# Optimization experiments

Hardware: AMD Instinct MI355X
Metric: run time of the kernel (lower is better)

The kernel has to match this reference:

```python
import jax, jax.numpy as jnp
import numpy as np

N_NODES = 50000
N_EDGES = 800000
D_FEAT = 128
D_HID = 500


def setup_inputs() -> dict:
    key = jax.random.key(0)
    k1, k2, k3, k4 = jax.random.split(key, 4)
    x = jax.random.normal(k1, (N_NODES, D_FEAT), dtype=jnp.float32)
    edge_index = jax.random.randint(k2, (2, N_EDGES), 0, N_NODES, dtype=jnp.int64)
    # Glorot-ish init for weights, zeros for bias (PyG GCNConv default)
    W1 = jax.random.normal(k3, (D_FEAT, D_HID), dtype=jnp.float32) / np.sqrt(D_FEAT)
    b1 = jnp.zeros((D_HID,), dtype=jnp.float32)
    W2 = jax.random.normal(k4, (D_HID, 1), dtype=jnp.float32) / np.sqrt(D_HID)
    b2 = jnp.zeros((1,), dtype=jnp.float32)
    return {"x": x, "edge_index": edge_index, "W1": W1, "b1": b1, "W2": W2, "b2": b2}


def gcn_conv(x, W, b, src, dst, n_nodes):
    """PyG GCNConv: linear transform, add self-loops, symmetric norm, scatter-add, bias."""
    h = x @ W  # [N, out]
    loops = jnp.arange(n_nodes, dtype=src.dtype)
    s = jnp.concatenate([src, loops])  # [E+N]
    d = jnp.concatenate([dst, loops])
    deg = jnp.zeros((n_nodes,), dtype=h.dtype).at[d].add(1.0)
    dinv = jnp.where(deg > 0, jax.lax.rsqrt(deg), 0.0)
    norm = dinv[s] * dinv[d]  # [E+N]
    msg = h[s] * norm[:, None]  # [E+N, out] -- dominant memory traffic
    out = jax.ops.segment_sum(msg, d, num_segments=n_nodes)
    return out + b


def reference(x, edge_index, W1, b1, W2, b2):
    src, dst = edge_index[0], edge_index[1]
    n = x.shape[0]
    h = gcn_conv(x, W1, b1, src, dst, n)
    h = jax.nn.relu(h)
    # F.dropout(training=self.training): identity in eval mode
    out = gcn_conv(h, W2, b2, src, dst, n)
    return out
```

## Files before the change

### kernel.cpp

```cpp
#include <hip/hip_runtime.h>


#define N_NODES 50000
#define N_EDGES 800000
#define D_FEAT  128
#define D_HID   500
#define NTILES  3125
#define RB2     1563
#define CSTRIDE 64

typedef __bf16 bf16x8 __attribute__((ext_vector_type(8)));
typedef float  f32x4  __attribute__((ext_vector_type(4)));

static __device__ inline unsigned int f2bf(float f) {
    unsigned int u = __float_as_uint(f);
    return (u + 0x7fffu + ((u >> 16) & 1u)) >> 16;
}
static __device__ inline float bf_lo(unsigned int u) { return __uint_as_float(u << 16); }
static __device__ inline float bf_hi(unsigned int u) { return __uint_as_float(u & 0xffff0000u); }

static __device__ inline void add8(float* acc, uint4 u) {
    acc[0] += bf_lo(u.x);
    acc[1] += bf_hi(u.x);
    acc[2] += bf_lo(u.y);
    acc[3] += bf_hi(u.y);
    acc[4] += bf_lo(u.z);
    acc[5] += bf_hi(u.z);
    acc[6] += bf_lo(u.w);
    acc[7] += bf_hi(u.w);
}

__global__ __launch_bounds__(256) void k_rank(const int* __restrict__ dst,
                                              const float* __restrict__ W1,
                                              const float* __restrict__ b1,
                                              const float* __restrict__ W2,
                                              int* __restrict__ deg,
                                              int* __restrict__ rank,
                                              unsigned short* __restrict__ b_pk,
                                              float* __restrict__ b1p,
                                              float* __restrict__ w2p) {
    const int b = blockIdx.x, tid = threadIdx.x;
    if (b < RB2) {
        int t2 = b * 256 + tid;
        if (t2 < N_EDGES / 2) {
            int e = t2 * 2;
            int2 d2 = *(const int2*)&dst[e];
            int2 r2;
            r2.x = atomicAdd(&deg[d2.x], 1);
            r2.y = atomicAdd(&deg[d2.y], 1);
            *(int2*)&rank[e] = r2;
        }
    } else if (b < RB2 + 32) {
        int idx  = (b - RB2) * 256 + tid;
        int lane = idx & 63;
        int slot = idx >> 6;
        int t    = slot >> 2;
        int ks   = slot & 3;
        int quad = lane >> 4;
        int n    = t * 16 + (lane & 15);
        unsigned int us[8];
#pragma unroll
        for (int j = 0; j < 8; j++) {
            int k = ks * 32 + quad * 8 + j;
            float v = (n < D_HID) ? W1[(size_t)k * D_HID + n] : 0.f;
            us[j] = f2bf(v);
        }
        uint4 p;
        p.x = us[0] | (us[1] << 16);
        p.y = us[2] | (us[3] << 16);
        p.z = us[4] | (us[5] << 16);
        p.w = us[6] | (us[7] << 16);
        ((uint4*)b_pk)[idx] = p;
    } else {
        for (int i = tid; i < 512; i += 256) {
            b1p[i] = (i < D_HID) ? b1[i] : 0.f;
            w2p[i] = (i < D_HID) ? W2[i] : 0.f;
        }
    }
}

__global__ __launch_bounds__(256) void k_fill(const int* __restrict__ src,
                                              const int* __restrict__ dst,
                                              const int* __restrict__ rank,
                                              const int* __restrict__ deg,
                                              const float* __restrict__ x,
                                              unsigned short* __restrict__ csrp,
                                              uint2* __restrict__ xd) {
    const int e = blockIdx.x * 256 + threadIdx.x;
    {
        int r = rank[e];
        if (r < CSTRIDE)
            csrp[dst[e] * CSTRIDE + r] = (unsigned short)src[e];
    }
    for (int i = e; i < N_NODES * D_FEAT / 4; i += N_EDGES) {
        float d = rsqrtf((float)(deg[i >> 5] + 1));
        float4 v = ((const float4*)x)[i];
        uint2 o;
        o.x = f2bf(d * v.x) | (f2bf(d * v.y) << 16);
        o.y = f2bf(d * v.z) | (f2bf(d * v.w) << 16);
        xd[i] = o;
    }
}

__global__ __launch_bounds__(256, 8) void k_gcn1(const uint4* __restrict__ xd4,
                                                 const unsigned short* __restrict__ csrp,
                                                 const int* __restrict__ deg,
                                                 const unsigned short* __restrict__ b_pk,
                                                 const float* __restrict__ b1p,
                                                 const float* __restrict__ w2p,
                                                 float* __restrict__ zd) {
    __shared__ unsigned short A[16][136];
    __shared__ float red[4][16];
    const int t = threadIdx.x;
    const int node0 = blockIdx.x * 16;
    const int wv = t >> 6, lane = t & 63;
    const int q = lane >> 4, p = lane & 15;

    {
        const int n = wv * 4 + q;
        const int node = node0 + n;
        int dg = deg[node];
        uint4 su = xd4[(size_t)node * 16 + p];
        if (dg > CSTRIDE) dg = CSTRIDE;
        const int base = node * CSTRIDE;
        float acc[8];
#pragma unroll
        for (int j = 0; j < 8; j++) acc[j] = 0.f;

        int e = 0;
        for (; e + 4 <= dg; e += 4) {
            ushort4 s4 = *(const ushort4*)&csrp[base + e];
            uint4 u0 = xd4[(size_t)s4.x * 16 + p];
            uint4 u1 = xd4[(size_t)s4.y * 16 + p];
            uint4 u2 = xd4[(size_t)s4.z * 16 + p];
            uint4 u3 = xd4[(size_t)s4.w * 16 + p];
            add8(acc, u0);
            add8(acc, u1);
            add8(acc, u2);
            add8(acc, u3);
        }
        for (; e < dg; e++) {
            int s = csrp[base + e];
            uint4 u = xd4[(size_t)s * 16 + p];
            add8(acc, u);
        }

        const float di = rsqrtf((float)(dg + 1));
        uint4 o;
        o.x = f2bf(di * (acc[0] + bf_lo(su.x))) |
              (f2bf(di * (acc[1] + bf_hi(su.x))) << 16);
        o.y = f2bf(di * (acc[2] + bf_lo(su.y))) |
              (f2bf(di * (acc[3] + bf_hi(su.y))) << 16);
        o.z = f2bf(di * (acc[4] + bf_lo(su.z))) |
              (f2bf(di * (acc[5] + bf_hi(su.z))) << 16);
        o.w = f2bf(di * (acc[6] + bf_lo(su.w))) |
              (f2bf(di * (acc[7] + bf_hi(su.w))) << 16);
        *(uint4*)&A[n][p * 8] = o;
    }
    __syncthreads();

    bf16x8 afr[4];
#pragma unroll
    for (int ks = 0; ks < 4; ks++)
        afr[ks] = *(const bf16x8*)&A[p][ks * 32 + q * 8];

    const bf16x8* __restrict__ bpk = (const bf16x8*)b_pk;
    f32x4 acc[8];
#pragma unroll
    for (int tt = 0; tt < 8; tt++) acc[tt] = (f32x4){0.f, 0.f, 0.f, 0.f};
#pragma unroll
    for (int tt = 0; tt < 8; tt++) {
        const int tile_n = wv * 8 + tt;
#pragma unroll
        for (int ks = 0; ks < 4; ks++) {
            bf16x8 bfr = bpk[(size_t)(tile_n * 4 + ks) * 64 + lane];
            acc[tt] = __builtin_amdgcn_mfma_f32_16x16x32_bf16(afr[ks], bfr, acc[tt], 0, 0, 0);
        }
    }

    float zp[4] = {0.f, 0.f, 0.f, 0.f};
#pragma unroll
    for (int tt = 0; tt < 8; tt++) {
        const int c = (wv * 8 + tt) * 16 + p;
        const float b1v = b1p[c];
        const float w2v = w2p[c];
#pragma unroll
        for (int r = 0; r < 4; r++)
            zp[r] += fmaxf(acc[tt][r] + b1v, 0.f) * w2v;
    }
#pragma unroll
    for (int off = 1; off < 16; off <<= 1) {
#pragma unroll
        for (int r = 0; r < 4; r++) zp[r] += __shfl_xor(zp[r], off);
    }
    if (p == 0) {
#pragma unroll
        for (int r = 0; r < 4; r++) red[wv][q * 4 + r] = zp[r];
    }
    __syncthreads();
    if (t < 16) {
        int node = node0 + t;
        float zz = red[0][t] + red[1][t] + red[2][t] + red[3][t];
        zd[node] = rsqrtf((float)(deg[node] + 1)) * zz;
    }
}

__global__ __launch_bounds__(256) void k_gz(const unsigned short* __restrict__ csrp,
                                            const int* __restrict__ deg,
                                            const float* __restrict__ zd,
                                            const float* __restrict__ b2,
                                            float* __restrict__ out) {
    const int node = blockIdx.x * 16 + (threadIdx.x >> 4);
    const int l = threadIdx.x & 15;
    int dg = deg[node];
    if (dg > CSTRIDE) dg = CSTRIDE;
    const int base = node * CSTRIDE;
    float s = 0.f;
    for (int e = l; e < dg; e += 16) s += zd[csrp[base + e]];
#pragma unroll
    for (int off = 1; off < 16; off <<= 1) s += __shfl_xor(s, off);
    if (l == 0) {
        float di = rsqrtf((float)(dg + 1));
        out[node] = di * (s + zd[node]) + b2[0];
    }
}

extern "C" void kernel_launch(void* const* d_in, const int* in_sizes, int n_in,
                              void* d_out, int out_size, void* d_ws, size_t ws_size,
                              hipStream_t stream) {
    const float* x  = (const float*)d_in[0];
    const int*   ei = (const int*)d_in[1];
    const float* W1 = (const float*)d_in[2];
    const float* b1 = (const float*)d_in[3];
    const float* W2 = (const float*)d_in[4];
    const float* b2 = (const float*)d_in[5];
    float* out = (float*)d_out;

    const int* src = ei;
    const int* dst = ei + N_EDGES;

    uint2* xd            = (uint2*)d_ws;
    unsigned short* b_pk = (unsigned short*)(xd + 1600000);
    float* b1p    = (float*)(b_pk + 65536);
    float* w2p    = b1p + 512;
    float* zd     = w2p + 512;
    int* deg      = (int*)(zd + N_NODES);
    int* rank     = deg + N_NODES;
    unsigned short* csrp = (unsigned short*)(rank + N_EDGES);

    hipMemsetAsync(deg, 0, N_NODES * sizeof(int), stream);

    k_rank<<<RB2 + 33, 256, 0, stream>>>(dst, W1, b1, W2, deg, rank,
                                         b_pk, b1p, w2p);
    k_fill<<<NTILES, 256, 0, stream>>>(src, dst, rank, deg, x, csrp, xd);
    k_gcn1<<<NTILES, 256, 0, stream>>>((const uint4*)xd, csrp, deg,
                                       b_pk, b1p, w2p, zd);
    k_gz  <<<NTILES, 256, 0, stream>>>(csrp, deg, zd, b2, out);
}
```

Baseline: 180.4 us.

## Move x-to-bf16 conversion into build kernel and apply source norm at gather

The bf16 conversion of x now runs in the first kernel on extra blocks alongside the degree atomics, instead of waiting for degrees in the fill kernel. Because x is no longer pre-scaled, the gather kernel loads a per-source dinv value and uses fused multiply-adds, and the self term uses di squared. Edge ranks are stored as clamped bytes rather than ints, which cuts rank write and read traffic. The trade-off is an extra small gather of dinv per edge and more FMAs in the aggregation loop.

```diff
diff --git a/kernel.cpp b/kernel.cpp
--- a/kernel.cpp
+++ b/kernel.cpp
@@ -7,6 +7,7 @@
 #define D_HID   500
 #define NTILES  3125
 #define RB2     1563
+#define CONVB   1563
 #define CSTRIDE 64
 
 typedef __bf16 bf16x8 __attribute__((ext_vector_type(8)));
@@ -19,39 +20,51 @@
 static __device__ inline float bf_lo(unsigned int u) { return __uint_as_float(u << 16); }
 static __device__ inline float bf_hi(unsigned int u) { return __uint_as_float(u & 0xffff0000u); }
 
-static __device__ inline void add8(float* acc, uint4 u) {
-    acc[0] += bf_lo(u.x);
-    acc[1] += bf_hi(u.x);
-    acc[2] += bf_lo(u.y);
-    acc[3] += bf_hi(u.y);
-    acc[4] += bf_lo(u.z);
-    acc[5] += bf_hi(u.z);
-    acc[6] += bf_lo(u.w);
-    acc[7] += bf_hi(u.w);
-}
-
-__global__ __launch_bounds__(256) void k_rank(const int* __restrict__ dst,
-                                              const float* __restrict__ W1,
-                                              const float* __restrict__ b1,
-                                              const float* __restrict__ W2,
-                                              int* __restrict__ deg,
-                                              int* __restrict__ rank,
-                                              unsigned short* __restrict__ b_pk,
-                                              float* __restrict__ b1p,
-                                              float* __restrict__ w2p) {
+static __device__ inline void fma8(float* acc, uint4 u, float d) {
+    acc[0] += d * bf_lo(u.x);
+    acc[1] += d * bf_hi(u.x);
+    acc[2] += d * bf_lo(u.y);
+    acc[3] += d * bf_hi(u.y);
+    acc[4] += d * bf_lo(u.z);
+    acc[5] += d * bf_hi(u.z);
+    acc[6] += d * bf_lo(u.w);
+    acc[7] += d * bf_hi(u.w);
+}
+
+__global__ __launch_bounds__(256) void k_build(const int* __restrict__ dst,
+                                               const float* __restrict__ x,
+                                               const float* __restrict__ W1,
+                                               const float* __restrict__ b1,
+                                               const float* __restrict__ W2,
+                                               int* __restrict__ deg,
+                                               unsigned char* __restrict__ rankb,
+                                               uint2* __restrict__ xr,
+                                               unsigned short* __restrict__ b_pk,
+                                               float* __restrict__ b1p,
+                                               float* __restrict__ w2p) {
     const int b = blockIdx.x, tid = threadIdx.x;
     if (b < RB2) {
         int t2 = b * 256 + tid;
         if (t2 < N_EDGES / 2) {
             int e = t2 * 2;
             int2 d2 = *(const int2*)&dst[e];
-            int2 r2;
-            r2.x = atomicAdd(&deg[d2.x], 1);
-            r2.y = atomicAdd(&deg[d2.y], 1);
-            *(int2*)&rank[e] = r2;
-        }
-    } else if (b < RB2 + 32) {
-        int idx  = (b - RB2) * 256 + tid;
+            int r0 = atomicAdd(&deg[d2.x], 1);
+            int r1 = atomicAdd(&deg[d2.y], 1);
+            unsigned int c0 = (r0 < 255) ? (unsigned int)r0 : 255u;
+            unsigned int c1 = (r1 < 255) ? (unsigned int)r1 : 255u;
+            ((unsigned short*)rankb)[t2] = (unsigned short)(c0 | (c1 << 8));
+        }
+    } else if (b < RB2 + CONVB) {
+        int i0 = (b - RB2) * 256 + tid;
+        for (int i = i0; i < N_NODES * D_FEAT / 4; i += CONVB * 256) {
+            float4 v = ((const float4*)x)[i];
+            uint2 o;
+            o.x = f2bf(v.x) | (f2bf(v.y) << 16);
+            o.y = f2bf(v.z) | (f2bf(v.w) << 16);
+            xr[i] = o;
+        }
+    } else if (b < RB2 + CONVB + 32) {
+        int idx  = (b - RB2 - CONVB) * 256 + tid;
         int lane = idx & 63;
         int slot = idx >> 6;
         int t    = slot >> 2;
@@ -81,30 +94,22 @@
 
 __global__ __launch_bounds__(256) void k_fill(const int* __restrict__ src,
                                               const int* __restrict__ dst,
-                                              const int* __restrict__ rank,
+                                              const unsigned char* __restrict__ rankb,
                                               const int* __restrict__ deg,
-                                              const float* __restrict__ x,
                                               unsigned short* __restrict__ csrp,
-                                              uint2* __restrict__ xd) {
+                                              float* __restrict__ dinv) {
     const int e = blockIdx.x * 256 + threadIdx.x;
-    {
-        int r = rank[e];
-        if (r < CSTRIDE)
-            csrp[dst[e] * CSTRIDE + r] = (unsigned short)src[e];
-    }
-    for (int i = e; i < N_NODES * D_FEAT / 4; i += N_EDGES) {
-        float d = rsqrtf((float)(deg[i >> 5] + 1));
-        float4 v = ((const float4*)x)[i];
-        uint2 o;
-        o.x = f2bf(d * v.x) | (f2bf(d * v.y) << 16);
-        o.y = f2bf(d * v.z) | (f2bf(d * v.w) << 16);
-        xd[i] = o;
-    }
+    int r = rankb[e];
+    if (r < CSTRIDE)
+        csrp[dst[e] * CSTRIDE + r] = (unsigned short)src[e];
+    if (e < N_NODES)
+        dinv[e] = rsqrtf((float)(deg[e] + 1));
 }
 
 __global__ __launch_bounds__(256, 8) void k_gcn1(const uint4* __restrict__ xd4,
                                                  const unsigned short* __restrict__ csrp,
                                                  const int* __restrict__ deg,
+                                                 const float* __restrict__ dinv,
                                                  const unsigned short* __restrict__ b_pk,
                                                  const float* __restrict__ b1p,
                                                  const float* __restrict__ w2p,
@@ -134,27 +139,32 @@
             uint4 u1 = xd4[(size_t)s4.y * 16 + p];
             uint4 u2 = xd4[(size_t)s4.z * 16 + p];
             uint4 u3 = xd4[(size_t)s4.w * 16 + p];
-            add8(acc, u0);
-            add8(acc, u1);
-            add8(acc, u2);
-            add8(acc, u3);
+            float d0 = dinv[s4.x];
+            float d1 = dinv[s4.y];
+            float d2 = dinv[s4.z];
+            float d3 = dinv[s4.w];
+            fma8(acc, u0, d0);
+            fma8(acc, u1, d1);
+            fma8(acc, u2, d2);
+            fma8(acc, u3, d3);
         }
         for (; e < dg; e++) {
             int s = csrp[base + e];
             uint4 u = xd4[(size_t)s * 16 + p];
-            add8(acc, u);
-        }
-
-        const float di = rsqrtf((float)(dg + 1));
+            fma8(acc, u, dinv[s]);
+        }
+
+        const float di  = rsqrtf((float)(dg + 1));
+        const float di2 = di * di;
         uint4 o;
-        o.x = f2bf(di * (acc[0] + bf_lo(su.x))) |
-              (f2bf(di * (acc[1] + bf_hi(su.x))) << 16);
-        o.y = f2bf(di * (acc[2] + bf_lo(su.y))) |
-              (f2bf(di * (acc[3] + bf_hi(su.y))) << 16);
-        o.z = f2bf(di * (acc[4] + bf_lo(su.z))) |
-              (f2bf(di * (acc[5] + bf_hi(su.z))) << 16);
-        o.w = f2bf(di * (acc[6] + bf_lo(su.w))) |
-              (f2bf(di * (acc[7] + bf_hi(su.w))) << 16);
+        o.x = f2bf(di * acc[0] + di2 * bf_lo(su.x)) |
+              (f2bf(di * acc[1] + di2 * bf_hi(su.x)) << 16);
+        o.y = f2bf(di * acc[2] + di2 * bf_lo(su.y)) |
+              (f2bf(di * acc[3] + di2 * bf_hi(su.y)) << 16);
+        o.z = f2bf(di * acc[4] + di2 * bf_lo(su.z)) |
+              (f2bf(di * acc[5] + di2 * bf_hi(su.z)) << 16);
+        o.w = f2bf(di * acc[6] + di2 * bf_lo(su.w)) |
+              (f2bf(di * acc[7] + di2 * bf_hi(su.w)) << 16);
         *(uint4*)&A[n][p * 8] = o;
     }
     __syncthreads();
@@ -239,21 +249,22 @@
     const int* src = ei;
     const int* dst = ei + N_EDGES;
 
-    uint2* xd            = (uint2*)d_ws;
-    unsigned short* b_pk = (unsigned short*)(xd + 1600000);
+    uint2* xr            = (uint2*)d_ws;
+    unsigned short* b_pk = (unsigned short*)(xr + 1600000);
     float* b1p    = (float*)(b_pk + 65536);
     float* w2p    = b1p + 512;
     float* zd     = w2p + 512;
     int* deg      = (int*)(zd + N_NODES);
-    int* rank     = deg + N_NODES;
-    unsigned short* csrp = (unsigned short*)(rank + N_EDGES);
+    float* dinv   = (float*)(deg + N_NODES);
+    unsigned short* csrp = (unsigned short*)(dinv + N_NODES);
+    unsigned char* rankb = (unsigned char*)(csrp + 3200000);
 
     hipMemsetAsync(deg, 0, N_NODES * sizeof(int), stream);
 
-    k_rank<<<RB2 + 33, 256, 0, stream>>>(dst, W1, b1, W2, deg, rank,
-                                         b_pk, b1p, w2p);
-    k_fill<<<NTILES, 256, 0, stream>>>(src, dst, rank, deg, x, csrp, xd);
-    k_gcn1<<<NTILES, 256, 0, stream>>>((const uint4*)xd, csrp, deg,
+    k_build<<<RB2 + CONVB + 33, 256, 0, stream>>>(dst, x, W1, b1, W2, deg,
+                                                  rankb, xr, b_pk, b1p, w2p);
+    k_fill<<<NTILES, 256, 0, stream>>>(src, dst, rankb, deg, csrp, dinv);
+    k_gcn1<<<NTILES, 256, 0, stream>>>((const uint4*)xr, csrp, deg, dinv,
                                        b_pk, b1p, w2p, zd);
     k_gz  <<<NTILES, 256, 0, stream>>>(csrp, deg, zd, b2, out);
 }
```

Result: no change. 182.9 us (+1.4%).

## Replace global atomic degree counting with per-block LDS histograms plus column scan

Applied to the files above, without the earlier changes.

Swaps the global atomicAdd degree/rank pass for 64 blocks that each build a packed 16-bit LDS histogram over a slice of edges, recording each edge's local rank. A new scan kernel turns the per-block counts into per-node offsets and the degree. The fill kernel then combines offset and local rank to place edges. This removes contended global atomics and the memset, but adds an extra kernel launch, a 64×N_NODES offset array in global memory, and only 64 blocks doing the histogram work, so parallelism in that pass is low.

```diff
diff --git a/kernel.cpp b/kernel.cpp
--- a/kernel.cpp
+++ b/kernel.cpp
@@ -6,7 +6,8 @@
 #define D_FEAT  128
 #define D_HID   500
 #define NTILES  3125
-#define RB2     1563
+#define BHIST   64
+#define EPB     12500
 #define CSTRIDE 64
 
 typedef __bf16 bf16x8 __attribute__((ext_vector_type(8)));
@@ -30,28 +31,32 @@
     acc[7] += bf_hi(u.w);
 }
 
-__global__ __launch_bounds__(256) void k_rank(const int* __restrict__ dst,
+__global__ __launch_bounds__(256) void k_hist(const int* __restrict__ dst,
                                               const float* __restrict__ W1,
                                               const float* __restrict__ b1,
                                               const float* __restrict__ W2,
-                                              int* __restrict__ deg,
-                                              int* __restrict__ rank,
+                                              unsigned short* __restrict__ coff,
+                                              unsigned short* __restrict__ lrank,
                                               unsigned short* __restrict__ b_pk,
                                               float* __restrict__ b1p,
                                               float* __restrict__ w2p) {
+    __shared__ unsigned int hist[N_NODES / 2];
     const int b = blockIdx.x, tid = threadIdx.x;
-    if (b < RB2) {
-        int t2 = b * 256 + tid;
-        if (t2 < N_EDGES / 2) {
-            int e = t2 * 2;
-            int2 d2 = *(const int2*)&dst[e];
-            int2 r2;
-            r2.x = atomicAdd(&deg[d2.x], 1);
-            r2.y = atomicAdd(&deg[d2.y], 1);
-            *(int2*)&rank[e] = r2;
-        }
-    } else if (b < RB2 + 32) {
-        int idx  = (b - RB2) * 256 + tid;
+    if (b < BHIST) {
+        for (int w = tid; w < N_NODES / 2; w += 256) hist[w] = 0u;
+        __syncthreads();
+        const int base = b * EPB;
+        for (int i = tid; i < EPB; i += 256) {
+            int d = dst[base + i];
+            unsigned int sh = (unsigned int)(d & 1) * 16u;
+            unsigned int old = atomicAdd(&hist[d >> 1], 1u << sh);
+            lrank[base + i] = (unsigned short)((old >> sh) & 0xffffu);
+        }
+        __syncthreads();
+        unsigned int* crow = (unsigned int*)coff + (size_t)b * (N_NODES / 2);
+        for (int w = tid; w < N_NODES / 2; w += 256) crow[w] = hist[w];
+    } else if (b < BHIST + 32) {
+        int idx  = (b - BHIST) * 256 + tid;
         int lane = idx & 63;
         int slot = idx >> 6;
         int t    = slot >> 2;
@@ -79,25 +84,43 @@
     }
 }
 
+__global__ __launch_bounds__(256) void k_scan(unsigned short* __restrict__ coff,
+                                              int* __restrict__ deg) {
+    const int n = blockIdx.x * 256 + threadIdx.x;
+    if (n >= N_NODES) return;
+    int run = 0;
+#pragma unroll 8
+    for (int b = 0; b < BHIST; b++) {
+        size_t idx = (size_t)b * N_NODES + n;
+        int c = coff[idx];
+        coff[idx] = (unsigned short)run;
+        run += c;
+    }
+    deg[n] = run;
+}
+
 __global__ __launch_bounds__(256) void k_fill(const int* __restrict__ src,
                                               const int* __restrict__ dst,
-                                              const int* __restrict__ rank,
+                                              const unsigned short* __restrict__ coff,
+                                              const unsigned short* __restrict__ lrank,
                                               const int* __restrict__ deg,
                                               const float* __restrict__ x,
                                               unsigned short* __restrict__ csrp,
                                               uint2* __restrict__ xd) {
     const int e = blockIdx.x * 256 + threadIdx.x;
     {
-        int r = rank[e];
+        int d = dst[e];
+        int b = e / EPB;
+        int r = (int)coff[(size_t)b * N_NODES + d] + (int)lrank[e];
         if (r < CSTRIDE)
-            csrp[dst[e] * CSTRIDE + r] = (unsigned short)src[e];
+            csrp[d * CSTRIDE + r] = (unsigned short)src[e];
     }
     for (int i = e; i < N_NODES * D_FEAT / 4; i += N_EDGES) {
-        float d = rsqrtf((float)(deg[i >> 5] + 1));
+        float dv = rsqrtf((float)(deg[i >> 5] + 1));
         float4 v = ((const float4*)x)[i];
         uint2 o;
-        o.x = f2bf(d * v.x) | (f2bf(d * v.y) << 16);
-        o.y = f2bf(d * v.z) | (f2bf(d * v.w) << 16);
+        o.x = f2bf(dv * v.x) | (f2bf(dv * v.y) << 16);
+        o.y = f2bf(dv * v.z) | (f2bf(dv * v.w) << 16);
         xd[i] = o;
     }
 }
@@ -245,14 +268,14 @@
     float* w2p    = b1p + 512;
     float* zd     = w2p + 512;
     int* deg      = (int*)(zd + N_NODES);
-    int* rank     = deg + N_NODES;
-    unsigned short* csrp = (unsigned short*)(rank + N_EDGES);
-
-    hipMemsetAsync(deg, 0, N_NODES * sizeof(int), stream);
-
-    k_rank<<<RB2 + 33, 256, 0, stream>>>(dst, W1, b1, W2, deg, rank,
-                                         b_pk, b1p, w2p);
-    k_fill<<<NTILES, 256, 0, stream>>>(src, dst, rank, deg, x, csrp, xd);
+    unsigned short* coff  = (unsigned short*)(deg + N_NODES);
+    unsigned short* lrank = coff + (size_t)BHIST * N_NODES;
+    unsigned short* csrp  = lrank + N_EDGES;
+
+    k_hist<<<BHIST + 33, 256, 0, stream>>>(dst, W1, b1, W2, coff, lrank,
+                                           b_pk, b1p, w2p);
+    k_scan<<<(N_NODES + 255) / 256, 256, 0, stream>>>(coff, deg);
+    k_fill<<<NTILES, 256, 0, stream>>>(src, dst, coff, lrank, deg, x, csrp, xd);
     k_gcn1<<<NTILES, 256, 0, stream>>>((const uint4*)xd, csrp, deg,
                                        b_pk, b1p, w2p, zd);
     k_gz  <<<NTILES, 256, 0, stream>>>(csrp, deg, zd, b2, out);
```

Measured after the change: 173.1 us. 4.0% less time.
